# Performance work log

Hardware: AMD Instinct MI355X
Metric: run time of the kernel (lower is better)

## Reference

```python
import jax, jax.numpy as jnp
import numpy as np

NUMS = 2048
DIM = 128

def setup_inputs() -> dict:
    key = jax.random.key(0)
    k1, k2 = jax.random.split(key)
    data = jax.random.normal(k1, (32, 512, DIM), dtype=jnp.float32)
    stdv = 1.0 / np.sqrt(DIM)
    weight = jax.random.uniform(k2, (NUMS, DIM), dtype=jnp.float32, minval=-stdv, maxval=stdv)
    return {"data": data, "weight": weight}

def reference(data, weight):
    b, t, d = data.shape
    nums = weight.shape[0]
    # attention scores: [b, t, nums]
    attention = jax.nn.sigmoid(jnp.einsum('btd,kd->btk', data, weight) / jnp.sqrt(jnp.asarray(d, data.dtype)))
    k_top = nums // 16 + 1  # 129
    topk_vals, _ = jax.lax.top_k(attention, k_top)  # [b, t, k_top]
    temporal_att = topk_vals.mean(axis=-1)          # [b, t]
    half = b // 2
    augment = jnp.einsum('btk,kd->btd', attention[:half], weight)  # [b//2, t, d]
    read_query = jnp.concatenate((data[:half], augment), axis=-1)  # [b//2, t, 2d]
    mem_score = 1.0 - temporal_att
    return (mem_score, read_query)
```

## Files before the change

### kernel.cpp

```cpp
#include <hip/hip_runtime.h>

typedef unsigned short u16;
typedef unsigned int u32;
typedef __attribute__((ext_vector_type(8))) short short8;
typedef __attribute__((ext_vector_type(4))) float floatx4;

#define NUMS 2048
#define DIM 128
#define ROWS_TOT 16384
#define HALF_ROWS 8192
#define KTOP 129
#define MTILE 16
#define SCALE 0.08838834764831845f

__device__ __forceinline__ u16 f2bf(float f) {
  u32 u = __builtin_bit_cast(u32, f);
  u += 0x7FFFu + ((u >> 16) & 1u);
  return (u16)(u >> 16);
}
__device__ __forceinline__ float bf2f(u16 b) {
  return __builtin_bit_cast(float, (u32)b << 16);
}

__global__ void cvt_data_k(const float* __restrict__ d, u16* __restrict__ db) {
  const int i = (blockIdx.x * 256 + threadIdx.x) * 8;
  const float4 a = *(const float4*)(d + i);
  const float4 b = *(const float4*)(d + i + 4);
  short8 v;
  v[0] = (short)f2bf(a.x); v[1] = (short)f2bf(a.y);
  v[2] = (short)f2bf(a.z); v[3] = (short)f2bf(a.w);
  v[4] = (short)f2bf(b.x); v[5] = (short)f2bf(b.y);
  v[6] = (short)f2bf(b.z); v[7] = (short)f2bf(b.w);
  *(short8*)(db + i) = v;
}

__global__ void cvt_w_k(const float* __restrict__ w, u16* __restrict__ wb,
                        u16* __restrict__ wt) {
  __shared__ u16 tile[32][33];
  const int tx = threadIdx.x, ty = threadIdx.y;
  const int x = blockIdx.x * 32 + tx;
  const int y0 = blockIdx.y * 32;
#pragma unroll
  for (int j = 0; j < 32; j += 8) {
    const u16 v = f2bf(w[(size_t)(y0 + ty + j) * DIM + x]);
    wb[(size_t)(y0 + ty + j) * DIM + x] = v;
    tile[ty + j][tx] = v;
  }
  __syncthreads();
  const int x2 = y0 + tx;
  const int y2 = blockIdx.x * 32 + ty;
#pragma unroll
  for (int j = 0; j < 32; j += 8)
    wt[(size_t)(y2 + j) * NUMS + x2] = tile[tx][ty + j];
}

__device__ __forceinline__ int s_idx(int r, int c) {
  return r * NUMS + ((((c >> 3) ^ r) << 3) | (c & 7));
}

__global__ __launch_bounds__(256, 2)
void fused_k(const u16* __restrict__ db, const u16* __restrict__ wb,
             const u16* __restrict__ wt, const float* __restrict__ dataF,
             float* __restrict__ out) {
  __shared__ u16 S[MTILE * NUMS];
  const int r0 = blockIdx.x * MTILE;
  const int lane = threadIdx.x & 63;
  const int wave = threadIdx.x >> 6;
  const int m = lane & 15;
  const int quad = lane >> 4;

  short8 afrag[4];
  {
    const u16* ap = db + (size_t)(r0 + m) * DIM + quad * 8;
#pragma unroll
    for (int ks = 0; ks < 4; ks++)
      afrag[ks] = *(const short8*)(ap + ks * 32);
  }
#pragma unroll 4
  for (int nt = 0; nt < 32; nt++) {
    const int n0 = wave * 512 + nt * 16;
    const u16* bp = wb + (size_t)(n0 + m) * DIM + quad * 8;
    floatx4 acc = {0.f, 0.f, 0.f, 0.f};
#pragma unroll
    for (int ks = 0; ks < 4; ks++) {
      short8 bfrag = *(const short8*)(bp + ks * 32);
      acc = __builtin_amdgcn_mfma_f32_16x16x32_bf16(afrag[ks], bfrag, acc, 0, 0, 0);
    }
    const int c = n0 + m;
#pragma unroll
    for (int reg = 0; reg < 4; reg++) {
      const int rr = quad * 4 + reg;
      float att = 1.f / (1.f + __expf(-acc[reg] * SCALE));
      att = fminf(fmaxf(att, 0.f), 1.f);
      S[s_idx(rr, c)] = f2bf(att);
    }
  }
  __syncthreads();

  if (r0 < HALF_ROWS) {
    {
      const int row = threadIdx.x >> 4;
      const int c8 = (threadIdx.x & 15) << 3;
      const float4* src = (const float4*)(dataF + (size_t)(r0 + row) * DIM + c8);
      float4* dst = (float4*)(out + 16384 + (size_t)(r0 + row) * 256 + c8);
      dst[0] = src[0];
      dst[1] = src[1];
    }
    const int n0 = wave * 32;
    floatx4 acc0 = {0.f, 0.f, 0.f, 0.f}, acc1 = {0.f, 0.f, 0.f, 0.f};
    const u16* w0 = wt + (size_t)(n0 + m) * NUMS + quad * 8;
    const u16* w1 = w0 + (size_t)16 * NUMS;
#pragma unroll 8
    for (int ks = 0; ks < 64; ks++) {
      const int chunk = ks * 4 + quad;
      short8 af = *(const short8*)(S + m * NUMS + ((chunk ^ m) << 3));
      short8 b0 = *(const short8*)(w0 + ks * 32);
      short8 b1 = *(const short8*)(w1 + ks * 32);
      acc0 = __builtin_amdgcn_mfma_f32_16x16x32_bf16(af, b0, acc0, 0, 0, 0);
      acc1 = __builtin_amdgcn_mfma_f32_16x16x32_bf16(af, b1, acc1, 0, 0, 0);
    }
#pragma unroll
    for (int reg = 0; reg < 4; reg++) {
      const int row = quad * 4 + reg;
      float* o = out + 16384 + (size_t)(r0 + row) * 256 + 128;
      o[n0 + m] = acc0[reg];
      o[n0 + 16 + m] = acc1[reg];
    }
  }

  for (int rr = wave * 4; rr < wave * 4 + 4; rr++) {
    float vals[32];
#pragma unroll
    for (int i = 0; i < 32; i++)
      vals[i] = bf2f(S[s_idx(rr, i * 64 + lane)]);

    auto count_ge = [&](float thr) {
      int cnt = 0;
#pragma unroll
      for (int i = 0; i < 32; i++) cnt += (vals[i] >= thr) ? 1 : 0;
#pragma unroll
      for (int off = 1; off < 64; off <<= 1) cnt += __shfl_xor(cnt, off);
      return cnt;
    };

    u32 lo = 0u, hi = 0x3F80u;
    if (count_ge(0.25f) >= KTOP) lo = 0x3E80u; else hi = 0x3E80u;
    while (hi - lo > 1u) {
      const u32 mid = (lo + hi) >> 1;
      if (count_ge(bf2f((u16)mid)) >= KTOP) lo = mid; else hi = mid;
    }
    const float vstar = bf2f((u16)lo);

    float s = 0.f;
    int cgt = 0;
#pragma unroll
    for (int i = 0; i < 32; i++) {
      if (vals[i] > vstar) { s += vals[i]; cgt++; }
    }
#pragma unroll
    for (int off = 1; off < 64; off <<= 1) {
      s += __shfl_xor(s, off);
      cgt += __shfl_xor(cgt, off);
    }
    if (lane == 0) {
      const float mean = (s + (float)(KTOP - cgt) * vstar) * (1.f / (float)KTOP);
      out[r0 + rr] = 1.f - mean;
    }
  }
}

extern "C" void kernel_launch(void* const* d_in, const int* in_sizes, int n_in,
                              void* d_out, int out_size, void* d_ws, size_t ws_size,
                              hipStream_t stream) {
  const float* data = (const float*)d_in[0];
  const float* weight = (const float*)d_in[1];
  float* out = (float*)d_out;

  u16* wt = (u16*)d_ws;
  u16* wb = wt + NUMS * DIM;
  u16* db = wb + NUMS * DIM;

  cvt_w_k<<<dim3(DIM / 32, NUMS / 32), dim3(32, 8), 0, stream>>>(weight, wb, wt);
  cvt_data_k<<<dim3(ROWS_TOT * DIM / (256 * 8)), dim3(256), 0, stream>>>(data, db);
  fused_k<<<dim3(ROWS_TOT / MTILE), dim3(256), 0, stream>>>(db, wb, wt, data, out);
}
```

Baseline: 191.5 us.

## Fuse data bf16 conversion into main kernel, use 512 threads, ballot-based top-k search

Drops the separate data-conversion kernel and converts fp32 data to bf16 fragments inside the fused kernel. Doubles the block to 8 waves so each wave handles half as many score tiles, augment columns and top-k rows. The threshold search now compares raw bf16 bit patterns and counts with ballot/popcount instead of shuffle reductions. It also seeds the search by evaluating 8 thresholds in a batch to narrow the range before bisecting. This removes a kernel launch and a global round-trip and cuts reduction latency, at the cost of more register pressure and a seed range that assumes where the 129th value usually falls.

After: 167.8 us. 1.14x faster.

```diff
diff --git a/kernel.cpp b/kernel.cpp
--- a/kernel.cpp
+++ b/kernel.cpp
@@ -2,6 +2,7 @@
 
 typedef unsigned short u16;
 typedef unsigned int u32;
+typedef unsigned long long u64;
 typedef __attribute__((ext_vector_type(8))) short short8;
 typedef __attribute__((ext_vector_type(4))) float floatx4;
 
@@ -18,20 +19,17 @@
   u += 0x7FFFu + ((u >> 16) & 1u);
   return (u16)(u >> 16);
 }
-__device__ __forceinline__ float bf2f(u16 b) {
-  return __builtin_bit_cast(float, (u32)b << 16);
+__device__ __forceinline__ float bf2f(u32 b) {
+  return __builtin_bit_cast(float, b << 16);
 }
 
-__global__ void cvt_data_k(const float* __restrict__ d, u16* __restrict__ db) {
-  const int i = (blockIdx.x * 256 + threadIdx.x) * 8;
-  const float4 a = *(const float4*)(d + i);
-  const float4 b = *(const float4*)(d + i + 4);
+__device__ __forceinline__ short8 pack_bf8(float4 a, float4 b) {
   short8 v;
   v[0] = (short)f2bf(a.x); v[1] = (short)f2bf(a.y);
   v[2] = (short)f2bf(a.z); v[3] = (short)f2bf(a.w);
   v[4] = (short)f2bf(b.x); v[5] = (short)f2bf(b.y);
   v[6] = (short)f2bf(b.z); v[7] = (short)f2bf(b.w);
-  *(short8*)(db + i) = v;
+  return v;
 }
 
 __global__ void cvt_w_k(const float* __restrict__ w, u16* __restrict__ wb,
@@ -58,27 +56,30 @@
   return r * NUMS + ((((c >> 3) ^ r) << 3) | (c & 7));
 }
 
-__global__ __launch_bounds__(256, 2)
-void fused_k(const u16* __restrict__ db, const u16* __restrict__ wb,
-             const u16* __restrict__ wt, const float* __restrict__ dataF,
-             float* __restrict__ out) {
+__global__ __launch_bounds__(512, 4)
+void fused_k(const float* __restrict__ dataF, const u16* __restrict__ wb,
+             const u16* __restrict__ wt, float* __restrict__ out) {
   __shared__ u16 S[MTILE * NUMS];
+  const int tid = threadIdx.x;
   const int r0 = blockIdx.x * MTILE;
-  const int lane = threadIdx.x & 63;
-  const int wave = threadIdx.x >> 6;
+  const int lane = tid & 63;
+  const int wave = tid >> 6;
   const int m = lane & 15;
   const int quad = lane >> 4;
 
   short8 afrag[4];
   {
-    const u16* ap = db + (size_t)(r0 + m) * DIM + quad * 8;
+    const float* ap = dataF + (size_t)(r0 + m) * DIM + quad * 8;
 #pragma unroll
-    for (int ks = 0; ks < 4; ks++)
-      afrag[ks] = *(const short8*)(ap + ks * 32);
+    for (int ks = 0; ks < 4; ks++) {
+      const float4 x = *(const float4*)(ap + ks * 32);
+      const float4 y = *(const float4*)(ap + ks * 32 + 4);
+      afrag[ks] = pack_bf8(x, y);
+    }
   }
 #pragma unroll 4
-  for (int nt = 0; nt < 32; nt++) {
-    const int n0 = wave * 512 + nt * 16;
+  for (int nt = 0; nt < 16; nt++) {
+    const int n0 = wave * 256 + nt * 16;
     const u16* bp = wb + (size_t)(n0 + m) * DIM + quad * 8;
     floatx4 acc = {0.f, 0.f, 0.f, 0.f};
 #pragma unroll
@@ -99,69 +100,73 @@
 
   if (r0 < HALF_ROWS) {
     {
-      const int row = threadIdx.x >> 4;
-      const int c8 = (threadIdx.x & 15) << 3;
-      const float4* src = (const float4*)(dataF + (size_t)(r0 + row) * DIM + c8);
-      float4* dst = (float4*)(out + 16384 + (size_t)(r0 + row) * 256 + c8);
-      dst[0] = src[0];
-      dst[1] = src[1];
+      const int row = tid >> 5;
+      const int c4 = (tid & 31) << 2;
+      *(float4*)(out + 16384 + (size_t)(r0 + row) * 256 + c4) =
+          *(const float4*)(dataF + (size_t)(r0 + row) * DIM + c4);
     }
-    const int n0 = wave * 32;
-    floatx4 acc0 = {0.f, 0.f, 0.f, 0.f}, acc1 = {0.f, 0.f, 0.f, 0.f};
+    const int n0 = wave * 16;
+    floatx4 acc = {0.f, 0.f, 0.f, 0.f};
     const u16* w0 = wt + (size_t)(n0 + m) * NUMS + quad * 8;
-    const u16* w1 = w0 + (size_t)16 * NUMS;
 #pragma unroll 8
     for (int ks = 0; ks < 64; ks++) {
       const int chunk = ks * 4 + quad;
       short8 af = *(const short8*)(S + m * NUMS + ((chunk ^ m) << 3));
       short8 b0 = *(const short8*)(w0 + ks * 32);
-      short8 b1 = *(const short8*)(w1 + ks * 32);
-      acc0 = __builtin_amdgcn_mfma_f32_16x16x32_bf16(af, b0, acc0, 0, 0, 0);
-      acc1 = __builtin_amdgcn_mfma_f32_16x16x32_bf16(af, b1, acc1, 0, 0, 0);
+      acc = __builtin_amdgcn_mfma_f32_16x16x32_bf16(af, b0, acc, 0, 0, 0);
     }
 #pragma unroll
     for (int reg = 0; reg < 4; reg++) {
       const int row = quad * 4 + reg;
-      float* o = out + 16384 + (size_t)(r0 + row) * 256 + 128;
-      o[n0 + m] = acc0[reg];
-      o[n0 + 16 + m] = acc1[reg];
+      out[16384 + (size_t)(r0 + row) * 256 + 128 + n0 + m] = acc[reg];
     }
   }
 
-  for (int rr = wave * 4; rr < wave * 4 + 4; rr++) {
-    float vals[32];
 #pragma unroll
-    for (int i = 0; i < 32; i++)
-      vals[i] = bf2f(S[s_idx(rr, i * 64 + lane)]);
+  for (int rv = 0; rv < 2; rv++) {
+    const int rr = wave * 2 + rv;
+    u32 bits[32];
+#pragma unroll
+    for (int j = 0; j < 4; j++) {
+      const short8 v = *(const short8*)(S + rr * NUMS + (j * 64 + lane) * 8);
+#pragma unroll
+      for (int t = 0; t < 8; t++) bits[j * 8 + t] = (u32)(u16)v[t];
+    }
 
-    auto count_ge = [&](float thr) {
-      int cnt = 0;
+    auto count_ge = [&](u32 t) -> int {
+      int c = 0;
 #pragma unroll
-      for (int i = 0; i < 32; i++) cnt += (vals[i] >= thr) ? 1 : 0;
-#pragma unroll
-      for (int off = 1; off < 64; off <<= 1) cnt += __shfl_xor(cnt, off);
-      return cnt;
+      for (int i = 0; i < 32; i++)
+        c += __popcll(__ballot(bits[i] >= t));
+      return c;
     };
 
-    u32 lo = 0u, hi = 0x3F80u;
-    if (count_ge(0.25f) >= KTOP) lo = 0x3E80u; else hi = 0x3E80u;
+    int cnt[8];
+#pragma unroll
+    for (int j = 0; j < 8; j++) cnt[j] = count_ge(0x3EE0u + ((u32)j << 4));
+    u32 lo = 0u, hi = 0x3F81u;
+#pragma unroll
+    for (int j = 0; j < 8; j++)
+      if (cnt[j] >= KTOP) lo = 0x3EE0u + ((u32)j << 4);
+#pragma unroll
+    for (int j = 7; j >= 0; j--)
+      if (cnt[j] < KTOP) hi = 0x3EE0u + ((u32)j << 4);
+
     while (hi - lo > 1u) {
       const u32 mid = (lo + hi) >> 1;
-      if (count_ge(bf2f((u16)mid)) >= KTOP) lo = mid; else hi = mid;
+      if (count_ge(mid) >= KTOP) lo = mid; else hi = mid;
     }
-    const float vstar = bf2f((u16)lo);
+    const float vstar = bf2f(lo);
 
     float s = 0.f;
     int cgt = 0;
 #pragma unroll
     for (int i = 0; i < 32; i++) {
-      if (vals[i] > vstar) { s += vals[i]; cgt++; }
+      if (bits[i] > lo) s += bf2f(bits[i]);
+      cgt += __popcll(__ballot(bits[i] > lo));
     }
 #pragma unroll
-    for (int off = 1; off < 64; off <<= 1) {
-      s += __shfl_xor(s, off);
-      cgt += __shfl_xor(cgt, off);
-    }
+    for (int off = 1; off < 64; off <<= 1) s += __shfl_xor(s, off);
     if (lane == 0) {
       const float mean = (s + (float)(KTOP - cgt) * vstar) * (1.f / (float)KTOP);
       out[r0 + rr] = 1.f - mean;
@@ -178,9 +183,7 @@
 
   u16* wt = (u16*)d_ws;
   u16* wb = wt + NUMS * DIM;
-  u16* db = wb + NUMS * DIM;
 
   cvt_w_k<<<dim3(DIM / 32, NUMS / 32), dim3(32, 8), 0, stream>>>(weight, wb, wt);
-  cvt_data_k<<<dim3(ROWS_TOT * DIM / (256 * 8)), dim3(256), 0, stream>>>(data, db);
-  fused_k<<<dim3(ROWS_TOT / MTILE), dim3(256), 0, stream>>>(db, wb, wt, data, out);
+  fused_k<<<dim3(ROWS_TOT / MTILE), dim3(512), 0, stream>>>(data, wb, wt, out);
 }
```
